# Performance work log

Measured on AMD Instinct MI355X. Metric: run time of the kernel, lower is better.

## Reference

```python
import jax, jax.numpy as jnp
import numpy as np

B, P, D = 64, 256, 768
S = P + 1            # class token + patches
GRID = 16.0          # sqrt(no_of_patches)
N_IMGS = 10000


def setup_inputs() -> dict:
    key = jax.random.key(0)
    ks = jax.random.split(key, 10)
    sc = 1.0 / np.sqrt(D)
    return {
        "x": jax.random.normal(ks[0], (B, S, D), jnp.float32),
        "img_ids": jax.random.randint(ks[1], (B,), 0, N_IMGS),
        "mask": jnp.ones((B, S), jnp.int32),
        "avgs": 0.1 * jax.random.normal(ks[2], (N_IMGS, 2, P), jnp.float32),
        "std_devs": jnp.ones((N_IMGS, 2, P), jnp.float32),
        "Wq": sc * jax.random.normal(ks[3], (D, D), jnp.float32),
        "bq": jnp.zeros((D,), jnp.float32),
        "Wk": sc * jax.random.normal(ks[4], (D, D), jnp.float32),
        "bk": jnp.zeros((D,), jnp.float32),
        "Wv": sc * jax.random.normal(ks[5], (D, D), jnp.float32),
        "bv": jnp.zeros((D,), jnp.float32),
        "noise_x": jax.random.normal(ks[6], (B, P), jnp.float32),  # torch.normal(0, sigma)
        "noise_y": jax.random.normal(ks[7], (B, P), jnp.float32),
    }


def reference(x, img_ids, mask, avgs, std_devs, Wq, bq, Wk, bk, Wv, bv, noise_x, noise_y):
    # nn.Linear: y = x @ W^T + b
    q = jnp.einsum("bsd,ed->bse", x, Wq) + bq  # (B,S,D)
    k = jnp.einsum("bsd,ed->bse", x, Wk) + bk
    v = jnp.einsum("bsd,ed->bse", x, Wv) + bv

    a = avgs[img_ids]       # (B,2,P)
    sd = std_devs[img_ids]  # (B,2,P)
    half = (GRID - 1.0) / 2.0
    kx = half * (1.0 + jnp.tanh((noise_x + a[:, 0]) * sd[:, 0]))  # (B,P) in (0, GRID-1)
    ky = half * (1.0 + jnp.tanh((noise_y + a[:, 1]) * sd[:, 1]))
    kx1, kx2 = jnp.ceil(kx), jnp.floor(kx)
    ky1, ky2 = jnp.ceil(ky), jnp.floor(ky)

    # corner order matches original: (x1,y1), (x2,y1), (x1,y2), (x2,y2)
    cx = jnp.stack([kx1, kx2, kx1, kx2], axis=1)  # (B,4,P)
    cy = jnp.stack([ky1, ky1, ky2, ky2], axis=1)
    idxs = jax.lax.stop_gradient(GRID * cy + cx).astype(jnp.int32)  # (B,4,P), < P

    sk = jnp.take_along_axis(k[:, None], idxs[..., None], axis=2)  # (B,4,P,D)
    sv = jnp.take_along_axis(v[:, None], idxs[..., None], axis=2)
    cls = jnp.ones((B, 4, 1, D), sk.dtype)
    skf = jnp.concatenate([cls, sk], axis=2)  # (B,4,S,D)
    svf = jnp.concatenate([cls, sv], axis=2)

    # score per query s against its 4 sampled corner keys; softmax over the 4 corners
    scores = jnp.einsum("bnsd,bsd->bsn", skf, q)   # (B,S,4)
    attn = jax.nn.softmax(scores, axis=-1)          # (B,S,4)
    attn_v = attn.transpose(0, 2, 1)[..., None] * svf  # (B,4,S,D)

    # bilinear weights (1-|cx-kx|)*(1-|cy-ky|); class-token weight fixed to 1
    w = (1.0 - jnp.abs(cx - kx[:, None])) * (1.0 - jnp.abs(cy - ky[:, None]))  # (B,4,P)
    wf = jnp.concatenate([jnp.ones((B, 4, 1), w.dtype), w], axis=2)  # (B,4,S)
    out = jnp.einsum("bns,bnsd->bsd", wf, attn_v)  # (B,S,D)
    return out
```

## Files before the change

kernel.cpp:

```cpp
#include <hip/hip_runtime.h>
#include <math.h>


typedef _Float16 f16x8 __attribute__((ext_vector_type(8)));
typedef _Float16 f16x4 __attribute__((ext_vector_type(4)));
typedef float    f32x4 __attribute__((ext_vector_type(4)));

#define MTOT 16448
#define DD   768
#define NC   2304
#define KT   12
#define MT   65
#define NT9  9
#define XU   (MT*KT*2048)
#define WU   (NT9*KT*2048)

__global__ __launch_bounds__(256) void prepass(
    const float* __restrict__ x,
    const float* __restrict__ Wq, const float* __restrict__ Wk, const float* __restrict__ Wv,
    _Float16* __restrict__ xp, _Float16* __restrict__ wp)
{
    const int gidx = blockIdx.x * 256 + threadIdx.x;
    const float* src;
    _Float16* dst;
    if (gidx < XU) {
        const int u = gidx & 2047, kt = (gidx >> 11) % KT, tile = gidx / (KT * 2048);
        const int lane = u & 63, ks = (u >> 6) & 1, mblk = u >> 7;
        int row = tile * 256 + mblk * 16 + (lane & 15);
        row = row < MTOT ? row : MTOT - 1;
        const int col = kt * 64 + ks * 32 + (lane >> 4) * 8;
        src = x + (size_t)row * DD + col;
        dst = xp + (size_t)gidx * 8;
    } else {
        const int g = gidx - XU;
        const int u = g & 2047, kt = (g >> 11) % KT, tile = g / (KT * 2048);
        const int lane = u & 63, ks = (u >> 6) & 1, mblk = u >> 7;
        const int wrow = tile * 256 + mblk * 16 + (lane & 15);
        const float* W = wrow < 768 ? Wq : (wrow < 1536 ? Wk : Wv);
        const int srow = wrow - (wrow < 768 ? 0 : (wrow < 1536 ? 768 : 1536));
        const int col = kt * 64 + ks * 32 + (lane >> 4) * 8;
        src = W + (size_t)srow * DD + col;
        dst = wp + (size_t)g * 8;
    }
    const float4 a = *(const float4*)src;
    const float4 b = *(const float4*)(src + 4);
    f16x8 o;
    o[0] = (_Float16)a.x; o[1] = (_Float16)a.y; o[2] = (_Float16)a.z; o[3] = (_Float16)a.w;
    o[4] = (_Float16)b.x; o[5] = (_Float16)b.y; o[6] = (_Float16)b.z; o[7] = (_Float16)b.w;
    *(f16x8*)dst = o;
}

#define GLD(srcp, ldsp) \
    __builtin_amdgcn_global_load_lds( \
        (const __attribute__((address_space(1))) void*)(srcp), \
        (__attribute__((address_space(3))) void*)(ldsp), 16, 0, 0)

__global__ __launch_bounds__(512, 1) void qkv_gemm(
    const _Float16* __restrict__ xp, const _Float16* __restrict__ wp,
    const float* __restrict__ bq, const float* __restrict__ bk, const float* __restrict__ bv,
    _Float16* __restrict__ qkv)
{
    __shared__ __align__(16) _Float16 Ax[2][16384];
    __shared__ __align__(16) _Float16 Bx[2][16384];

    const int bid = blockIdx.x;
    const int xcd = bid & 7, pos = bid >> 3;
    const int orig = (xcd == 0) ? pos : 74 + (xcd - 1) * 73 + pos;
    const int tileM = orig / NT9, tileN = orig % NT9;

    const int tid = threadIdx.x, lane = tid & 63, wid = tid >> 6;
    const int wm = wid >> 2, wn = wid & 3;
    const int r16 = lane & 15, kq = lane >> 4;

    const _Float16* Asrc = xp + (size_t)tileM * KT * 2048 * 8;
    const _Float16* Bsrc = wp + (size_t)tileN * KT * 2048 * 8;

    const f32x4 zero = {0.f, 0.f, 0.f, 0.f};
    f32x4 acc[8][4];
    #pragma unroll
    for (int i = 0; i < 8; ++i)
        #pragma unroll
        for (int j = 0; j < 4; ++j) acc[i][j] = zero;

    #pragma unroll
    for (int g = 0; g < 4; ++g) {
        const int c0 = g * 512 + wid * 64;
        GLD(Asrc + (size_t)(c0 + lane) * 8, &Ax[0][c0 * 8]);
        GLD(Bsrc + (size_t)(c0 + lane) * 8, &Bx[0][c0 * 8]);
    }
    asm volatile("s_waitcnt vmcnt(0)" ::: "memory");
    __builtin_amdgcn_sched_barrier(0);
    __builtin_amdgcn_s_barrier();
    __builtin_amdgcn_sched_barrier(0);

    for (int t = 0; t < KT; ++t) {
        const int cur = t & 1;
        if (t + 1 < KT) {
            const size_t off = (size_t)(t + 1) * 2048;
            #pragma unroll
            for (int g = 0; g < 4; ++g) {
                const int c0 = g * 512 + wid * 64;
                GLD(Asrc + (off + c0 + lane) * 8, &Ax[cur ^ 1][c0 * 8]);
                GLD(Bsrc + (off + c0 + lane) * 8, &Bx[cur ^ 1][c0 * 8]);
            }
        }
        __builtin_amdgcn_sched_barrier(0);

        f16x8 bf[4][2];
        #pragma unroll
        for (int j = 0; j < 4; ++j)
            #pragma unroll
            for (int ks = 0; ks < 2; ++ks)
                bf[j][ks] = *(const f16x8*)(&Bx[cur][(((wn * 4 + j) * 2 + ks) * 64 + lane) * 8]);
        {
            f16x8 aa[4][2];
            #pragma unroll
            for (int i = 0; i < 4; ++i)
                #pragma unroll
                for (int ks = 0; ks < 2; ++ks)
                    aa[i][ks] = *(const f16x8*)(&Ax[cur][(((wm * 8 + i) * 2 + ks) * 64 + lane) * 8]);
            __builtin_amdgcn_s_setprio(1);
            #pragma unroll
            for (int i = 0; i < 4; ++i)
                #pragma unroll
                for (int j = 0; j < 4; ++j)
                    #pragma unroll
                    for (int ks = 0; ks < 2; ++ks)
                        acc[i][j] = __builtin_amdgcn_mfma_f32_16x16x32_f16(aa[i][ks], bf[j][ks], acc[i][j], 0, 0, 0);
            __builtin_amdgcn_s_setprio(0);
        }
        {
            f16x8 aa[4][2];
            #pragma unroll
            for (int i = 0; i < 4; ++i)
                #pragma unroll
                for (int ks = 0; ks < 2; ++ks)
                    aa[i][ks] = *(const f16x8*)(&Ax[cur][(((wm * 8 + 4 + i) * 2 + ks) * 64 + lane) * 8]);
            __builtin_amdgcn_s_setprio(1);
            #pragma unroll
            for (int i = 0; i < 4; ++i)
                #pragma unroll
                for (int j = 0; j < 4; ++j)
                    #pragma unroll
                    for (int ks = 0; ks < 2; ++ks)
                        acc[4 + i][j] = __builtin_amdgcn_mfma_f32_16x16x32_f16(aa[i][ks], bf[j][ks], acc[4 + i][j], 0, 0, 0);
            __builtin_amdgcn_s_setprio(0);
        }

        asm volatile("s_waitcnt vmcnt(0) lgkmcnt(0)" ::: "memory");
        __builtin_amdgcn_sched_barrier(0);
        __builtin_amdgcn_s_barrier();
        __builtin_amdgcn_sched_barrier(0);
    }

    const float* bias = tileN < 3 ? bq : (tileN < 6 ? bk : bv);
    const int bcolbase = (tileN % 3) * 256 + wn * 64;
    #pragma unroll
    for (int i = 0; i < 8; ++i) {
        const int row0 = tileM * 256 + wm * 128 + i * 16 + kq * 4;
        #pragma unroll
        for (int j = 0; j < 4; ++j) {
            const int col = tileN * 256 + wn * 64 + j * 16 + r16;
            const float bb = bias[bcolbase + j * 16 + r16];
            #pragma unroll
            for (int tt = 0; tt < 4; ++tt) {
                const int row = row0 + tt;
                if (row < MTOT)
                    qkv[(size_t)row * NC + col] = (_Float16)(acc[i][j][tt] + bb);
            }
        }
    }
}

__global__ __launch_bounds__(256) void attn_gather(
    const _Float16* __restrict__ qkv,
    const int*   __restrict__ ids,
    const float* __restrict__ avgs,
    const float* __restrict__ stds,
    const float* __restrict__ nx,
    const float* __restrict__ ny,
    float* __restrict__ out)
{
    const int tid  = threadIdx.x;
    const int lane = tid & 63;
    const int bid = blockIdx.x;
    const int swz = (bid & 7) * 514 + (bid >> 3);
    const int gid = swz * 4 + (tid >> 6);
    const int b = gid / 257, s = gid % 257;
    float* orow = out + (size_t)gid * DD;

    if (s == 0) {
        const float4 one = make_float4(1.f, 1.f, 1.f, 1.f);
        #pragma unroll
        for (int j = 0; j < 3; ++j)
            *(float4*)(orow + 4 * lane + 256 * j) = one;
        return;
    }
    const int p   = s - 1;
    const int img = ids[b];
    const size_t ab = (size_t)img * 512 + p;
    const float a0 = avgs[ab], a1 = avgs[ab + 256];
    const float s0 = stds[ab], s1 = stds[ab + 256];
    const float kx = 7.5f * (1.f + tanhf((nx[b * 256 + p] + a0) * s0));
    const float ky = 7.5f * (1.f + tanhf((ny[b * 256 + p] + a1) * s1));
    const float kx1 = ceilf(kx), kx2 = floorf(kx);
    const float ky1 = ceilf(ky), ky2 = floorf(ky);
    const float cx[4] = {kx1, kx2, kx1, kx2};
    const float cy[4] = {ky1, ky1, ky2, ky2};
    int   idx[4];
    float w[4];
    #pragma unroll
    for (int n = 0; n < 4; ++n) {
        idx[n] = (int)(16.f * cy[n] + cx[n]);
        w[n]   = (1.f - fabsf(cx[n] - kx)) * (1.f - fabsf(cy[n] - ky));
    }

    const _Float16* qrow = qkv + (size_t)gid * NC;
    float qf[12];
    #pragma unroll
    for (int j = 0; j < 3; ++j) {
        const f16x4 v = *(const f16x4*)(qrow + lane * 4 + j * 256);
        qf[4 * j + 0] = (float)v[0]; qf[4 * j + 1] = (float)v[1];
        qf[4 * j + 2] = (float)v[2]; qf[4 * j + 3] = (float)v[3];
    }

    float sc[4];
    #pragma unroll
    for (int n = 0; n < 4; ++n) {
        const _Float16* krow = qkv + (size_t)(b * 257 + idx[n]) * NC + 768;
        float a = 0.f;
        #pragma unroll
        for (int j = 0; j < 3; ++j) {
            const f16x4 kv = *(const f16x4*)(krow + lane * 4 + j * 256);
            a += qf[4 * j + 0] * (float)kv[0] + qf[4 * j + 1] * (float)kv[1]
               + qf[4 * j + 2] * (float)kv[2] + qf[4 * j + 3] * (float)kv[3];
        }
        sc[n] = a;
    }
    #pragma unroll
    for (int n = 0; n < 4; ++n)
        for (int off = 32; off > 0; off >>= 1)
            sc[n] += __shfl_xor(sc[n], off);

    const float mx = fmaxf(fmaxf(sc[0], sc[1]), fmaxf(sc[2], sc[3]));
    const float e0 = expf(sc[0] - mx), e1 = expf(sc[1] - mx),
                e2 = expf(sc[2] - mx), e3 = expf(sc[3] - mx);
    const float inv = 1.f / (e0 + e1 + e2 + e3);
    const float coef[4] = {e0 * inv * w[0], e1 * inv * w[1], e2 * inv * w[2], e3 * inv * w[3]};

    const _Float16* vr0 = qkv + (size_t)(b * 257 + idx[0]) * NC + 1536;
    const _Float16* vr1 = qkv + (size_t)(b * 257 + idx[1]) * NC + 1536;
    const _Float16* vr2 = qkv + (size_t)(b * 257 + idx[2]) * NC + 1536;
    const _Float16* vr3 = qkv + (size_t)(b * 257 + idx[3]) * NC + 1536;
    #pragma unroll
    for (int j = 0; j < 3; ++j) {
        const int d = lane * 4 + j * 256;
        const f16x4 v0 = *(const f16x4*)(vr0 + d);
        const f16x4 v1 = *(const f16x4*)(vr1 + d);
        const f16x4 v2 = *(const f16x4*)(vr2 + d);
        const f16x4 v3 = *(const f16x4*)(vr3 + d);
        float4 o;
        o.x = coef[0] * (float)v0[0] + coef[1] * (float)v1[0] + coef[2] * (float)v2[0] + coef[3] * (float)v3[0];
        o.y = coef[0] * (float)v0[1] + coef[1] * (float)v1[1] + coef[2] * (float)v2[1] + coef[3] * (float)v3[1];
        o.z = coef[0] * (float)v0[2] + coef[1] * (float)v1[2] + coef[2] * (float)v2[2] + coef[3] * (float)v3[2];
        o.w = coef[0] * (float)v0[3] + coef[1] * (float)v1[3] + coef[2] * (float)v2[3] + coef[3] * (float)v3[3];
        *(float4*)(orow + d) = o;
    }
}

extern "C" void kernel_launch(void* const* d_in, const int* in_sizes, int n_in,
                              void* d_out, int out_size, void* d_ws, size_t ws_size,
                              hipStream_t stream) {
    const float* x    = (const float*)d_in[0];
    const int*   ids  = (const int*)  d_in[1];
    const float* avgs = (const float*)d_in[3];
    const float* stds = (const float*)d_in[4];
    const float* Wq   = (const float*)d_in[5];
    const float* bq   = (const float*)d_in[6];
    const float* Wk   = (const float*)d_in[7];
    const float* bk   = (const float*)d_in[8];
    const float* Wv   = (const float*)d_in[9];
    const float* bv   = (const float*)d_in[10];
    const float* nx   = (const float*)d_in[11];
    const float* ny   = (const float*)d_in[12];
    float* out = (float*)d_out;

    char* ws = (char*)d_ws;
    _Float16* qkv = (_Float16*)ws;
    _Float16* xp  = (_Float16*)(ws + 75792384);
    _Float16* wp  = (_Float16*)(ws + 75792384 + 25559040);

    prepass<<<(XU + WU) / 256, 256, 0, stream>>>(x, Wq, Wk, Wv, xp, wp);
    qkv_gemm<<<585, 512, 0, stream>>>(xp, wp, bq, bk, bv, qkv);
    attn_gather<<<4112, 256, 0, stream>>>(qkv, ids, avgs, stds, nx, ny, out);
}
```

Measured before the change: 140.0 us.

## Restructure QKV GEMM main loop into fine-grained interleaved load/MFMA phases

Rewrites the K-loop of the QKV GEMM as a two-tile unrolled, 8-phase schedule. Each phase issues a half-tile of global-to-LDS loads, reads A/B fragments from LDS, and runs a 4x2 MFMA block between barriers. B for the next tile is prefetched ahead of A, with partial vmcnt waits in place of a full drain per tile. The aim is to overlap memory traffic with MFMA work and cut the per-tile stall, at the cost of many more barriers and tight dependence on correct wait counts.

```diff
diff --git a/kernel.cpp b/kernel.cpp
--- a/kernel.cpp
+++ b/kernel.cpp
@@ -55,6 +55,36 @@
         (const __attribute__((address_space(1))) void*)(srcp), \
         (__attribute__((address_space(3))) void*)(ldsp), 16, 0, 0)
 
+#define PH_SYNC_IN do { \
+    __builtin_amdgcn_sched_barrier(0); \
+    __builtin_amdgcn_s_barrier(); \
+    asm volatile("s_waitcnt lgkmcnt(0)" ::: "memory"); \
+    __builtin_amdgcn_sched_barrier(0); } while (0)
+
+#define PH_SYNC_OUT do { \
+    __builtin_amdgcn_sched_barrier(0); \
+    __builtin_amdgcn_s_barrier(); \
+    __builtin_amdgcn_sched_barrier(0); } while (0)
+
+#define RD_A(dst, base, c) { \
+    _Pragma("unroll") for (int i = 0; i < 4; ++i) { \
+        _Pragma("unroll") for (int ks = 0; ks < 2; ++ks) \
+            dst[i][ks] = *(const f16x8*)(&Ax[c][(((wm*8 + (base) + i)*2 + ks)*64 + lane)*8]); } }
+
+#define RD_B(dst, base, c) { \
+    _Pragma("unroll") for (int j = 0; j < 2; ++j) { \
+        _Pragma("unroll") for (int ks = 0; ks < 2; ++ks) \
+            dst[j][ks] = *(const f16x8*)(&Bx[c][(((wn*4 + (base) + j)*2 + ks)*64 + lane)*8]); } }
+
+#define MM16(av, bv, io, jo) { \
+    __builtin_amdgcn_s_setprio(1); \
+    _Pragma("unroll") for (int i = 0; i < 4; ++i) { \
+        _Pragma("unroll") for (int j = 0; j < 2; ++j) { \
+            _Pragma("unroll") for (int ks = 0; ks < 2; ++ks) \
+                acc[(io)+i][(jo)+j] = __builtin_amdgcn_mfma_f32_16x16x32_f16( \
+                    av[i][ks], bv[j][ks], acc[(io)+i][(jo)+j], 0, 0, 0); } } \
+    __builtin_amdgcn_s_setprio(0); }
+
 __global__ __launch_bounds__(512, 1) void qkv_gemm(
     const _Float16* __restrict__ xp, const _Float16* __restrict__ wp,
     const float* __restrict__ bq, const float* __restrict__ bk, const float* __restrict__ bv,
@@ -72,8 +102,25 @@
     const int wm = wid >> 2, wn = wid & 3;
     const int r16 = lane & 15, kq = lane >> 4;
 
-    const _Float16* Asrc = xp + (size_t)tileM * KT * 2048 * 8;
-    const _Float16* Bsrc = wp + (size_t)tileN * KT * 2048 * 8;
+    const _Float16* Asrc = xp + (size_t)tileM * KT * 16384;
+    const _Float16* Bsrc = wp + (size_t)tileN * KT * 16384;
+
+    auto stA = [&](int t, int half) {
+        const _Float16* s = Asrc + ((size_t)t * 2048 + half * 1024) * 8;
+        #pragma unroll
+        for (int l = 0; l < 2; ++l) {
+            const int u = l * 512 + tid;
+            GLD(s + (size_t)u * 8, &Ax[t & 1][(half * 1024 + u) * 8]);
+        }
+    };
+    auto stB = [&](int t, int half) {
+        const _Float16* s = Bsrc + ((size_t)t * 2048 + half * 1024) * 8;
+        #pragma unroll
+        for (int l = 0; l < 2; ++l) {
+            const int u = l * 512 + tid;
+            GLD(s + (size_t)u * 8, &Bx[t & 1][(half * 1024 + u) * 8]);
+        }
+    };
 
     const f32x4 zero = {0.f, 0.f, 0.f, 0.f};
     f32x4 acc[8][4];
@@ -82,75 +129,48 @@
         #pragma unroll
         for (int j = 0; j < 4; ++j) acc[i][j] = zero;
 
-    #pragma unroll
-    for (int g = 0; g < 4; ++g) {
-        const int c0 = g * 512 + wid * 64;
-        GLD(Asrc + (size_t)(c0 + lane) * 8, &Ax[0][c0 * 8]);
-        GLD(Bsrc + (size_t)(c0 + lane) * 8, &Bx[0][c0 * 8]);
-    }
-    asm volatile("s_waitcnt vmcnt(0)" ::: "memory");
+    stA(0, 0); stA(0, 1); stB(0, 0); stB(0, 1);
+    stB(1, 0); stB(1, 1);
+    asm volatile("s_waitcnt vmcnt(4)" ::: "memory");
     __builtin_amdgcn_sched_barrier(0);
     __builtin_amdgcn_s_barrier();
     __builtin_amdgcn_sched_barrier(0);
 
-    for (int t = 0; t < KT; ++t) {
-        const int cur = t & 1;
-        if (t + 1 < KT) {
-            const size_t off = (size_t)(t + 1) * 2048;
-            #pragma unroll
-            for (int g = 0; g < 4; ++g) {
-                const int c0 = g * 512 + wid * 64;
-                GLD(Asrc + (off + c0 + lane) * 8, &Ax[cur ^ 1][c0 * 8]);
-                GLD(Bsrc + (off + c0 + lane) * 8, &Bx[cur ^ 1][c0 * 8]);
-            }
-        }
-        __builtin_amdgcn_sched_barrier(0);
-
-        f16x8 bf[4][2];
-        #pragma unroll
-        for (int j = 0; j < 4; ++j)
-            #pragma unroll
-            for (int ks = 0; ks < 2; ++ks)
-                bf[j][ks] = *(const f16x8*)(&Bx[cur][(((wn * 4 + j) * 2 + ks) * 64 + lane) * 8]);
-        {
-            f16x8 aa[4][2];
-            #pragma unroll
-            for (int i = 0; i < 4; ++i)
-                #pragma unroll
-                for (int ks = 0; ks < 2; ++ks)
-                    aa[i][ks] = *(const f16x8*)(&Ax[cur][(((wm * 8 + i) * 2 + ks) * 64 + lane) * 8]);
-            __builtin_amdgcn_s_setprio(1);
-            #pragma unroll
-            for (int i = 0; i < 4; ++i)
-                #pragma unroll
-                for (int j = 0; j < 4; ++j)
-                    #pragma unroll
-                    for (int ks = 0; ks < 2; ++ks)
-                        acc[i][j] = __builtin_amdgcn_mfma_f32_16x16x32_f16(aa[i][ks], bf[j][ks], acc[i][j], 0, 0, 0);
-            __builtin_amdgcn_s_setprio(0);
-        }
-        {
-            f16x8 aa[4][2];
-            #pragma unroll
-            for (int i = 0; i < 4; ++i)
-                #pragma unroll
-                for (int ks = 0; ks < 2; ++ks)
-                    aa[i][ks] = *(const f16x8*)(&Ax[cur][(((wm * 8 + 4 + i) * 2 + ks) * 64 + lane) * 8]);
-            __builtin_amdgcn_s_setprio(1);
-            #pragma unroll
-            for (int i = 0; i < 4; ++i)
-                #pragma unroll
-                for (int j = 0; j < 4; ++j)
-                    #pragma unroll
-                    for (int ks = 0; ks < 2; ++ks)
-                        acc[4 + i][j] = __builtin_amdgcn_mfma_f32_16x16x32_f16(aa[i][ks], bf[j][ks], acc[4 + i][j], 0, 0, 0);
-            __builtin_amdgcn_s_setprio(0);
-        }
-
-        asm volatile("s_waitcnt vmcnt(0) lgkmcnt(0)" ::: "memory");
-        __builtin_amdgcn_sched_barrier(0);
-        __builtin_amdgcn_s_barrier();
-        __builtin_amdgcn_sched_barrier(0);
+    #pragma unroll 1
+    for (int it = 0; it < KT / 2; ++it) {
+        const int t0 = 2 * it;
+        const bool g2 = (t0 + 2 < KT), g3 = (t0 + 3 < KT);
+        f16x8 a03[4][2], a47[4][2], b01[2][2], b23[2][2];
+
+        RD_A(a03, 0, 0); RD_B(b01, 0, 0);
+        stA(t0 + 1, 0);
+        PH_SYNC_IN; MM16(a03, b01, 0, 0); PH_SYNC_OUT;
+        RD_B(b23, 2, 0);
+        stA(t0 + 1, 1);
+        PH_SYNC_IN; MM16(a03, b23, 0, 2); PH_SYNC_OUT;
+        RD_A(a47, 4, 0);
+        if (g2) stB(t0 + 2, 0);
+        PH_SYNC_IN; MM16(a47, b23, 4, 2); PH_SYNC_OUT;
+        if (g2) {
+            stB(t0 + 2, 1);
+            asm volatile("s_waitcnt vmcnt(4)" ::: "memory");
+        } else {
+            asm volatile("s_waitcnt vmcnt(0)" ::: "memory");
+        }
+        PH_SYNC_IN; MM16(a47, b01, 4, 0); PH_SYNC_OUT;
+
+        RD_A(a03, 0, 1); RD_B(b01, 0, 1);
+        if (g2) stA(t0 + 2, 0);
+        PH_SYNC_IN; MM16(a03, b01, 0, 0); PH_SYNC_OUT;
+        RD_B(b23, 2, 1);
+        if (g2) stA(t0 + 2, 1);
+        PH_SYNC_IN; MM16(a03, b23, 0, 2); PH_SYNC_OUT;
+        RD_A(a47, 4, 1);
+        if (g3) stB(t0 + 3, 0);
+        PH_SYNC_IN; MM16(a47, b23, 4, 2); PH_SYNC_OUT;
+        if (g3) stB(t0 + 3, 1);
+        asm volatile("s_waitcnt vmcnt(4)" ::: "memory");
+        PH_SYNC_IN; MM16(a47, b01, 4, 0); PH_SYNC_OUT;
     }
 
     const float* bias = tileN < 3 ? bq : (tileN < 6 ? bk : bv);
```

Result: slower. 149.1 us (+6.6%).
